# Kernel optimization log

Hardware: AMD Instinct MI355X
Metric: run time of the kernel (lower is better)

Reference implementation:

```python
import jax, jax.numpy as jnp
import numpy as np

L1_COST = 1000.0
ENTROPY_COST = 5e-05


def setup_inputs() -> dict:
    key = jax.random.key(0)
    k1, k2 = jax.random.split(key)
    inputs = jax.random.normal(k1, (8, 4096, 256), dtype=jnp.float32)
    # xavier_uniform for [K, D]: bound = sqrt(6/(K+D))
    K, D = 1024, 256
    bound = np.sqrt(6.0 / (K + D)).astype(np.float32)
    codebook = jax.random.uniform(k2, (K, D), dtype=jnp.float32, minval=-bound, maxval=bound)
    return {"inputs": inputs, "codebook": codebook}


def reference(inputs, codebook):
    D = codebook.shape[1]
    flat = inputs.reshape(-1, D)                                  # [N, D]
    norm_C = codebook / jnp.linalg.norm(codebook, axis=1, keepdims=True)   # [K, D]
    flat = flat / jnp.linalg.norm(flat, axis=1, keepdims=True)    # [N, D]
    distances = jax.nn.softmax(flat @ norm_C.T, axis=1)           # [N, K]
    reconstruction = (distances @ norm_C).reshape(inputs.shape)   # [B, S, D]
    # l1_loss(distances, zeros) == mean(|distances|)
    l1 = jnp.mean(jnp.abs(distances))
    # entropy term: mean_i sum_k [ -log_softmax(distances) @ distances.T ]_{ik}
    # = mean_i ( -log_softmax(distances)_i . colsum(distances) ), an O(N*K) equivalent
    log_sm = jax.nn.log_softmax(distances, axis=1)                # [N, K]
    col_sum = jnp.sum(distances, axis=0)                          # [K]
    entropy = jnp.mean(-(log_sm @ col_sum))
    loss = L1_COST * l1 + ENTROPY_COST * entropy
    return reconstruction, loss
```

## Files before the change

### kernel.cpp

```cpp
#include <hip/hip_runtime.h>
#include <cstdint>

#define N_ROWS 32768
#define KDIM 1024
#define DDIM 256

typedef __attribute__((ext_vector_type(8))) short bf16x8;
typedef __attribute__((ext_vector_type(4))) float f32x4;

__device__ __forceinline__ unsigned short f2bf(float f) {
  unsigned int u = __float_as_uint(f);
  u += 0x7FFFu + ((u >> 16) & 1u);
  return (unsigned short)(u >> 16);
}
__device__ __forceinline__ float bf2f(unsigned short b) {
  return __uint_as_float((unsigned int)b << 16);
}

__device__ __forceinline__ void gload_lds16(const void* g, void* l) {
  __builtin_amdgcn_global_load_lds(
      (const __attribute__((address_space(1))) unsigned int*)(uintptr_t)g,
      (__attribute__((address_space(3))) unsigned int*)(unsigned int)(uintptr_t)l,
      16, 0, 0);
}


__global__ __launch_bounds__(256) void k_norm_cb(const float* __restrict__ cb,
                                                 unsigned short* __restrict__ Cn,
                                                 unsigned short* __restrict__ CnT,
                                                 float* __restrict__ m_g) {
  __shared__ float msh[4][256];
  const int wid = threadIdx.x >> 6, lane = threadIdx.x & 63;
  const int k = blockIdx.x * 4 + wid;
  float4 v = ((const float4*)(cb + (size_t)k * DDIM))[lane];
  float s = v.x * v.x + v.y * v.y + v.z * v.z + v.w * v.w;
#pragma unroll
  for (int m = 32; m; m >>= 1) s += __shfl_xor(s, m, 64);
  const float rn = 1.0f / sqrtf(s);
  ushort4 p;
  p.x = f2bf(v.x * rn); p.y = f2bf(v.y * rn);
  p.z = f2bf(v.z * rn); p.w = f2bf(v.w * rn);
  const int kb = lane >> 3;
  const int physA = ((lane & 7) >> 1) ^ (k & 3);
  *(ushort4*)(Cn + (size_t)(k >> 6) * 16384 + kb * 2048 + (k & 63) * 32 + physA * 8 + (lane & 1) * 4) = p;
  const int sgl = k >> 5, c31 = k & 31, ch = c31 >> 3, cw = c31 & 7;
  const unsigned short pv[4] = {p.x, p.y, p.z, p.w};
#pragma unroll
  for (int j = 0; j < 4; ++j) {
    const int d = lane * 4 + j;
    CnT[(size_t)sgl * 8192 + d * 32 + ((ch ^ j) * 8) + cw] = pv[j];
    msh[wid][d] = bf2f(pv[j]);
  }
  __syncthreads();
  const int tid = threadIdx.x;
  if (tid < 256) atomicAdd(&m_g[tid], msh[0][tid] + msh[1][tid] + msh[2][tid] + msh[3][tid]);
}

__global__ __launch_bounds__(256) void k_gram(const unsigned short* __restrict__ CnT,
                                              unsigned short* __restrict__ Mn) {
  __shared__ unsigned short T[2][8192];
  const int tid = threadIdx.x, wv = tid >> 6, lane = tid & 63;
  const int l15 = lane & 15, l4 = lane >> 4;
  const int ab = blockIdx.x;
  const int xsw = l4 ^ (l15 & 3);
  f32x4 acc[4] = {};
#pragma unroll
  for (int i = 0; i < 4; ++i) {
    const int o = i * 2048 + tid * 8;
    gload_lds16(CnT + o, (char*)T[0] + (size_t)o * 2);
  }
  for (int ks = 0; ks < 32; ++ks) {
    __syncthreads();
    if (ks < 31) {
#pragma unroll
      for (int i = 0; i < 4; ++i) {
        const int o = i * 2048 + tid * 8;
        gload_lds16(CnT + (size_t)(ks + 1) * 8192 + o, (char*)T[(ks + 1) & 1] + (size_t)o * 2);
      }
    }
    const unsigned short* B = T[ks & 1];
    bf16x8 a = *(const bf16x8*)&B[(ab * 16 + l15) * 32 + xsw * 8];
#pragma unroll
    for (int ni = 0; ni < 4; ++ni) {
      const int d = wv * 64 + ni * 16 + l15;
      bf16x8 b = *(const bf16x8*)&B[d * 32 + xsw * 8];
      acc[ni] = __builtin_amdgcn_mfma_f32_16x16x32_bf16(a, b, acc[ni], 0, 0, 0);
    }
  }
#pragma unroll
  for (int ni = 0; ni < 4; ++ni)
#pragma unroll
    for (int reg = 0; reg < 4; ++reg) {
      const int a_ = ab * 16 + l4 * 4 + reg;
      const int b_ = wv * 64 + ni * 16 + l15;
      Mn[(size_t)(b_ >> 6) * 16384 + (a_ >> 5) * 2048 + (b_ & 63) * 32 +
         ((((a_ & 31) >> 3) ^ (b_ & 3)) * 8) + (a_ & 7)] = f2bf(acc[ni][reg]);
    }
}

__global__ __launch_bounds__(512, 2) void k_all(const float* __restrict__ x,
                                                const unsigned short* __restrict__ Cn,
                                                const unsigned short* __restrict__ CnT,
                                                const unsigned short* __restrict__ Mn,
                                                const float* __restrict__ m_g,
                                                float* __restrict__ colsum_g,
                                                float* __restrict__ accL,
                                                int* __restrict__ cnt2,
                                                float* __restrict__ out) {
  __shared__ unsigned short Cb[4][16384];
  __shared__ unsigned short Ps[128 * 72];
  __shared__ float csl[1024];
  __shared__ float u_sh[128], t_sh[128], irl[128];
  __shared__ float lse_sh[2];
  __shared__ float sh1[4], sh2[4];
  __shared__ int lastf;

  const int tid = threadIdx.x, wid = tid >> 6, lane = tid & 63;
  const int l15 = lane & 15, l4 = lane >> 4;
  const int wm = wid >> 1, wn = wid & 1;
  const int rb = blockIdx.x;
  if (tid < 128) t_sh[tid] = 0.f;
  for (int j = tid; j < 1024; j += 512) csl[j] = 0.f;

#define STAGE32(SRC, DST)                                          \
  do {                                                             \
    _Pragma("unroll") for (int i_ = 0; i_ < 4; ++i_) {             \
      const int off_ = i_ * 8192 + wid * 1024 + lane * 16;         \
      gload_lds16((const char*)(SRC) + off_, (char*)(DST) + off_); \
    }                                                              \
  } while (0)

  STAGE32(Mn, Cb[2]);
  STAGE32((const char*)Mn + 32768, Cb[3]);

  unsigned short* Xs = &Cb[0][0];
  const float4 mv = ((const float4*)m_g)[lane];
#pragma unroll
  for (int p16 = 0; p16 < 16; ++p16) {
    const int row = p16 * 8 + wid;
    float4 v = ((const float4*)(x + (size_t)(rb * 128 + row) * DDIM))[lane];
    float s = v.x * v.x + v.y * v.y + v.z * v.z + v.w * v.w;
#pragma unroll
    for (int m = 32; m; m >>= 1) s += __shfl_xor(s, m, 64);
    const float rn = 1.0f / sqrtf(s);
    ushort4 p;
    p.x = f2bf(v.x * rn); p.y = f2bf(v.y * rn);
    p.z = f2bf(v.z * rn); p.w = f2bf(v.w * rn);
    *(ushort4*)&Xs[(lane >> 3) * 4096 + row * 32 + (lane & 7) * 4] = p;
    float ud = bf2f(p.x) * mv.x + bf2f(p.y) * mv.y + bf2f(p.z) * mv.z + bf2f(p.w) * mv.w;
#pragma unroll
    for (int m = 32; m; m >>= 1) ud += __shfl_xor(ud, m, 64);
    if (lane == 0) u_sh[row] = ud;
  }
  __syncthreads();
  bf16x8 areg[2][8];
#pragma unroll
  for (int mi = 0; mi < 2; ++mi)
#pragma unroll
    for (int kb = 0; kb < 8; ++kb)
      areg[mi][kb] = *(const bf16x8*)&Xs[kb * 4096 + (wm * 32 + mi * 16 + l15) * 32 + l4 * 8];

  const int xsw = l4 ^ (l15 & 3);

  float tacc[2][4] = {{0.f, 0.f, 0.f, 0.f}, {0.f, 0.f, 0.f, 0.f}};
  auto t_step = [&](const unsigned short* Sm, int bbase) {
    f32x4 Y[2][2] = {};
#pragma unroll
    for (int kb = 0; kb < 8; ++kb) {
      bf16x8 b0 = *(const bf16x8*)&Sm[kb * 2048 + (wn * 32 + l15) * 32 + xsw * 8];
      bf16x8 b1 = *(const bf16x8*)&Sm[kb * 2048 + (wn * 32 + 16 + l15) * 32 + xsw * 8];
#pragma unroll
      for (int mi = 0; mi < 2; ++mi) {
        Y[mi][0] = __builtin_amdgcn_mfma_f32_16x16x32_bf16(areg[mi][kb], b0, Y[mi][0], 0, 0, 0);
        Y[mi][1] = __builtin_amdgcn_mfma_f32_16x16x32_bf16(areg[mi][kb], b1, Y[mi][1], 0, 0, 0);
      }
    }
#pragma unroll
    for (int mi = 0; mi < 2; ++mi)
#pragma unroll
      for (int ni = 0; ni < 2; ++ni) {
        const int b = bbase + wn * 32 + ni * 16 + l15;
#pragma unroll
        for (int reg = 0; reg < 4; ++reg) {
          const int row = wm * 32 + mi * 16 + l4 * 4 + reg;
          const float xv = bf2f(Xs[(b >> 5) * 4096 + row * 32 + (b & 31)]);
          tacc[mi][reg] += Y[mi][ni][reg] * xv;
        }
      }
  };
  t_step(Cb[2], 0);
  __syncthreads();
  STAGE32((const char*)Mn + 65536, Cb[2]);
  t_step(Cb[3], 64);
  __syncthreads();
  STAGE32((const char*)Mn + 98304, Cb[3]);
  t_step(Cb[2], 128);
  __syncthreads();
  STAGE32(Cn, Cb[2]);
  t_step(Cb[3], 192);
  __syncthreads();
  STAGE32(CnT, Cb[3]);

#pragma unroll
  for (int mi = 0; mi < 2; ++mi)
#pragma unroll
    for (int reg = 0; reg < 4; ++reg) {
#pragma unroll
      for (int m = 1; m < 16; m <<= 1) tacc[mi][reg] += __shfl_xor(tacc[mi][reg], m, 64);
    }
  if (l15 == 0) {
#pragma unroll
    for (int mi = 0; mi < 2; ++mi)
#pragma unroll
      for (int reg = 0; reg < 4; ++reg)
        atomicAdd(&t_sh[wm * 32 + mi * 16 + l4 * 4 + reg], tacc[mi][reg]);
  }
  __syncthreads();
  if (tid < 128) {
    const float uu = u_sh[tid], tt = t_sh[tid];
    const float r = (float)KDIM + uu + 0.5f * tt;
    const float ir = 1.0f / r;
    irl[tid] = ir;
    const float q = (float)KDIM + 2.0f * uu + 2.0f * tt;
    float lse = logf((float)(KDIM + 1) + 0.5f * q * ir * ir);
#pragma unroll
    for (int m = 32; m; m >>= 1) lse += __shfl_xor(lse, m, 64);
    if ((tid & 63) == 0) lse_sh[tid >> 6] = lse;
  }
  __syncthreads();
  if (tid == 0) atomicAdd(accL, lse_sh[0] + lse_sh[1]);
  f32x4 ir2[2];
#pragma unroll
  for (int mi = 0; mi < 2; ++mi)
    ir2[mi] = *(const f32x4*)&irl[wm * 32 + mi * 16 + l4 * 4];

  f32x4 O[2][8] = {};
  const int psw_r = l15 >> 1;
  for (int kt = 0; kt < 16; ++kt) {
    const int cslot = (kt & 1) ? 0 : 2;
    const int tslot = cslot | 1;
    const int nslot = (kt & 1) ? 2 : 0;
    if (kt < 15) STAGE32((const char*)Cn + (size_t)(kt + 1) * 32768, Cb[nslot]);
    f32x4 S[2][2] = {};
#pragma unroll
    for (int kb = 0; kb < 8; ++kb) {
      bf16x8 b[2];
#pragma unroll
      for (int ni = 0; ni < 2; ++ni)
        b[ni] = *(const bf16x8*)&Cb[cslot][kb * 2048 + (wn * 32 + ni * 16 + l15) * 32 + xsw * 8];
#pragma unroll
      for (int mi = 0; mi < 2; ++mi)
#pragma unroll
        for (int ni = 0; ni < 2; ++ni)
          S[mi][ni] = __builtin_amdgcn_mfma_f32_16x16x32_bf16(areg[mi][kb], b[ni], S[mi][ni], 0, 0, 0);
    }
    float cs[2] = {0.f, 0.f};
#pragma unroll
    for (int mi = 0; mi < 2; ++mi)
#pragma unroll
      for (int reg = 0; reg < 4; ++reg) {
        const int row = wm * 32 + mi * 16 + l4 * 4 + reg;
        const int pswz = (l4 * 2 + (reg >> 1)) & 7;
#pragma unroll
        for (int ni = 0; ni < 2; ++ni) {
          const float e = __expf(S[mi][ni][reg]);
          const int chl = wn * 4 + ni * 2 + (l15 >> 3);
          Ps[row * 72 + ((chl ^ pswz) * 8) + (l15 & 7)] = f2bf(e);
          cs[ni] += e * ir2[mi][reg];
        }
      }
#pragma unroll
    for (int ni = 0; ni < 2; ++ni) {
      float v = cs[ni];
      v += __shfl_xor(v, 16, 64);
      v += __shfl_xor(v, 32, 64);
      if (lane < 16) atomicAdd(&csl[kt * 64 + wn * 32 + ni * 16 + l15], v);
    }
    __syncthreads();
    if (kt < 15) STAGE32((const char*)CnT + (size_t)(kt + 1) * 32768, Cb[nslot + 1]);
#pragma unroll
    for (int kb2 = 0; kb2 < 2; ++kb2) {
      bf16x8 a2[2], b2[8];
#pragma unroll
      for (int mi = 0; mi < 2; ++mi) {
        const int row = wm * 32 + mi * 16 + l15;
        a2[mi] = *(const bf16x8*)&Ps[row * 72 + (((kb2 * 4 + l4) ^ psw_r) * 8)];
      }
#pragma unroll
      for (int ni = 0; ni < 8; ++ni) {
        const int d = wn * 128 + ni * 16 + l15;
        b2[ni] = *(const bf16x8*)&Cb[tslot][kb2 * 8192 + d * 32 + xsw * 8];
      }
#pragma unroll
      for (int mi = 0; mi < 2; ++mi)
#pragma unroll
        for (int ni = 0; ni < 8; ++ni)
          O[mi][ni] = __builtin_amdgcn_mfma_f32_16x16x32_bf16(a2[mi], b2[ni], O[mi][ni], 0, 0, 0);
    }
    __syncthreads();
  }

#pragma unroll
  for (int mi = 0; mi < 2; ++mi)
#pragma unroll
    for (int reg = 0; reg < 4; ++reg) {
      const int row = wm * 32 + mi * 16 + l4 * 4 + reg;
      const float irv = ir2[mi][reg];
#pragma unroll
      for (int ni = 0; ni < 8; ++ni) {
        const int d = wn * 128 + ni * 16 + l15;
        out[(size_t)(rb * 128 + row) * DDIM + d] = O[mi][ni][reg] * irv;
      }
    }
  for (int j = tid; j < 1024; j += 512) atomicAdd(&colsum_g[j], csl[j]);

  if (tid == 0) {
    __threadfence();
    const int old = __hip_atomic_fetch_add(cnt2, 1, __ATOMIC_ACQ_REL, __HIP_MEMORY_SCOPE_AGENT);
    lastf = (old == 255);
  }
  __syncthreads();
  if (lastf) {
    if (tid < 256) {
      float s = 0.f, q = 0.f;
#pragma unroll
      for (int j = 0; j < 4; ++j) {
        const float c = __hip_atomic_load(&colsum_g[tid + j * 256], __ATOMIC_RELAXED, __HIP_MEMORY_SCOPE_AGENT);
        s += c; q += c * c;
      }
#pragma unroll
      for (int m = 1; m < 64; m <<= 1) {
        s += __shfl_xor(s, m, 64);
        q += __shfl_xor(q, m, 64);
      }
      if (lane == 0) { sh1[tid >> 6] = s; sh2[tid >> 6] = q; }
    }
    __syncthreads();
    if (tid == 0) {
      const double S = (double)sh1[0] + sh1[1] + sh1[2] + sh1[3];
      const double Q = (double)sh2[0] + sh2[1] + sh2[2] + sh2[3];
      const double L = __hip_atomic_load(accL, __ATOMIC_RELAXED, __HIP_MEMORY_SCOPE_AGENT);
      const double entropy = (S * L - Q) / (double)N_ROWS;
      const double l1 = S / ((double)N_ROWS * (double)KDIM);
      out[(size_t)N_ROWS * DDIM] = (float)(1000.0 * l1 + 5e-5 * entropy);
    }
  }
#undef STAGE32
}

extern "C" void kernel_launch(void* const* d_in, const int* in_sizes, int n_in,
                              void* d_out, int out_size, void* d_ws, size_t ws_size,
                              hipStream_t stream) {
  const float* x = (const float*)d_in[0];
  const float* cb = (const float*)d_in[1];
  float* out = (float*)d_out;
  char* ws = (char*)d_ws;

  unsigned short* Cn  = (unsigned short*)(ws + 0);
  unsigned short* CnT = (unsigned short*)(ws + 524288);
  unsigned short* Mn  = (unsigned short*)(ws + 1048576);
  float* colsum_g     = (float*)(ws + 1179648);
  float* m_g          = (float*)(ws + 1183744);
  float* accL         = (float*)(ws + 1184768);
  int* cnt2           = (int*)(ws + 1184772);

  hipMemsetAsync(ws + 1179648, 0, 5128, stream);
  k_norm_cb<<<256, 256, 0, stream>>>(cb, Cn, CnT, m_g);
  k_gram<<<16, 256, 0, stream>>>(CnT, Mn);
  k_all<<<256, 512, 0, stream>>>(x, Cn, CnT, Mn, m_g, colsum_g, accL, cnt2, out);
}
```

Measured before the change: 185.2 us.

## Replace __syncthreads with partial vmcnt waits and deepen async prefetch pipelines

In the gram kernel, the LDS ring grows from two to four slots and three stages are prefetched ahead, with explicit s_waitcnt vmcnt counts so only the oldest load is awaited. In the main kernel, full __syncthreads barriers become raw s_barrier calls with targeted vmcnt/lgkmcnt waits. The CnT stage is issued together with the Cn stage one step earlier so both loads overlap the whole iteration, and the accL atomic moves to the end. This is meant to cut load stalls caused by draining all outstanding memory operations at each barrier, at the risk of race bugs if the hand-counted vmcnt values do not match the number of loads actually in flight.

Result: no change. 182.9 us (-1.2%).

```diff
diff --git a/kernel.cpp b/kernel.cpp
--- a/kernel.cpp
+++ b/kernel.cpp
@@ -58,27 +58,27 @@
 
 __global__ __launch_bounds__(256) void k_gram(const unsigned short* __restrict__ CnT,
                                               unsigned short* __restrict__ Mn) {
-  __shared__ unsigned short T[2][8192];
+  __shared__ unsigned short T[4][8192];
   const int tid = threadIdx.x, wv = tid >> 6, lane = tid & 63;
   const int l15 = lane & 15, l4 = lane >> 4;
   const int ab = blockIdx.x;
   const int xsw = l4 ^ (l15 & 3);
   f32x4 acc[4] = {};
-#pragma unroll
-  for (int i = 0; i < 4; ++i) {
-    const int o = i * 2048 + tid * 8;
-    gload_lds16(CnT + o, (char*)T[0] + (size_t)o * 2);
-  }
+#define STAGE_T(KS, SLOT)                                                            \
+  do {                                                                               \
+    _Pragma("unroll") for (int i_ = 0; i_ < 4; ++i_) {                               \
+      const int o_ = i_ * 2048 + tid * 8;                                            \
+      gload_lds16(CnT + (size_t)(KS) * 8192 + o_, (char*)T[SLOT] + (size_t)o_ * 2);  \
+    }                                                                                \
+  } while (0)
+  STAGE_T(0, 0); STAGE_T(1, 1); STAGE_T(2, 2);
   for (int ks = 0; ks < 32; ++ks) {
-    __syncthreads();
-    if (ks < 31) {
-#pragma unroll
-      for (int i = 0; i < 4; ++i) {
-        const int o = i * 2048 + tid * 8;
-        gload_lds16(CnT + (size_t)(ks + 1) * 8192 + o, (char*)T[(ks + 1) & 1] + (size_t)o * 2);
-      }
-    }
-    const unsigned short* B = T[ks & 1];
+    if (ks <= 29)      asm volatile("s_waitcnt vmcnt(8)" ::: "memory");
+    else if (ks == 30) asm volatile("s_waitcnt vmcnt(4)" ::: "memory");
+    else               asm volatile("s_waitcnt vmcnt(0)" ::: "memory");
+    __builtin_amdgcn_s_barrier();
+    __builtin_amdgcn_sched_barrier(0);
+    const unsigned short* B = T[ks & 3];
     bf16x8 a = *(const bf16x8*)&B[(ab * 16 + l15) * 32 + xsw * 8];
 #pragma unroll
     for (int ni = 0; ni < 4; ++ni) {
@@ -86,7 +86,11 @@
       bf16x8 b = *(const bf16x8*)&B[d * 32 + xsw * 8];
       acc[ni] = __builtin_amdgcn_mfma_f32_16x16x32_bf16(a, b, acc[ni], 0, 0, 0);
     }
-  }
+    __builtin_amdgcn_s_barrier();
+    __builtin_amdgcn_sched_barrier(0);
+    if (ks <= 28) STAGE_T(ks + 3, (ks + 3) & 3);
+  }
+#undef STAGE_T
 #pragma unroll
   for (int ni = 0; ni < 4; ++ni)
 #pragma unroll
@@ -189,16 +193,22 @@
       }
   };
   t_step(Cb[2], 0);
-  __syncthreads();
+  __builtin_amdgcn_s_barrier();
+  __builtin_amdgcn_sched_barrier(0);
   STAGE32((const char*)Mn + 65536, Cb[2]);
   t_step(Cb[3], 64);
-  __syncthreads();
+  asm volatile("s_waitcnt vmcnt(0)" ::: "memory");
+  __builtin_amdgcn_s_barrier();
+  __builtin_amdgcn_sched_barrier(0);
   STAGE32((const char*)Mn + 98304, Cb[3]);
   t_step(Cb[2], 128);
-  __syncthreads();
+  asm volatile("s_waitcnt vmcnt(0)" ::: "memory");
+  __builtin_amdgcn_s_barrier();
+  __builtin_amdgcn_sched_barrier(0);
   STAGE32(Cn, Cb[2]);
   t_step(Cb[3], 192);
-  __syncthreads();
+  __builtin_amdgcn_s_barrier();
+  __builtin_amdgcn_sched_barrier(0);
   STAGE32(CnT, Cb[3]);
 
 #pragma unroll
@@ -215,7 +225,8 @@
       for (int reg = 0; reg < 4; ++reg)
         atomicAdd(&t_sh[wm * 32 + mi * 16 + l4 * 4 + reg], tacc[mi][reg]);
   }
-  __syncthreads();
+  asm volatile("s_waitcnt lgkmcnt(0)" ::: "memory");
+  __builtin_amdgcn_s_barrier();
   if (tid < 128) {
     const float uu = u_sh[tid], tt = t_sh[tid];
     const float r = (float)KDIM + uu + 0.5f * tt;
@@ -227,12 +238,15 @@
     for (int m = 32; m; m >>= 1) lse += __shfl_xor(lse, m, 64);
     if ((tid & 63) == 0) lse_sh[tid >> 6] = lse;
   }
-  __syncthreads();
-  if (tid == 0) atomicAdd(accL, lse_sh[0] + lse_sh[1]);
+  asm volatile("s_waitcnt lgkmcnt(0)" ::: "memory");
+  __builtin_amdgcn_s_barrier();
   f32x4 ir2[2];
 #pragma unroll
   for (int mi = 0; mi < 2; ++mi)
     ir2[mi] = *(const f32x4*)&irl[wm * 32 + mi * 16 + l4 * 4];
+  asm volatile("s_waitcnt vmcnt(4)" ::: "memory");
+  __builtin_amdgcn_s_barrier();
+  __builtin_amdgcn_sched_barrier(0);
 
   f32x4 O[2][8] = {};
   const int psw_r = l15 >> 1;
@@ -240,7 +254,10 @@
     const int cslot = (kt & 1) ? 0 : 2;
     const int tslot = cslot | 1;
     const int nslot = (kt & 1) ? 2 : 0;
-    if (kt < 15) STAGE32((const char*)Cn + (size_t)(kt + 1) * 32768, Cb[nslot]);
+    if (kt < 15) {
+      STAGE32((const char*)Cn + (size_t)(kt + 1) * 32768, Cb[nslot]);
+      STAGE32((const char*)CnT + (size_t)(kt + 1) * 32768, Cb[nslot + 1]);
+    }
     f32x4 S[2][2] = {};
 #pragma unroll
     for (int kb = 0; kb < 8; ++kb) {
@@ -276,8 +293,10 @@
       v += __shfl_xor(v, 32, 64);
       if (lane < 16) atomicAdd(&csl[kt * 64 + wn * 32 + ni * 16 + l15], v);
     }
-    __syncthreads();
-    if (kt < 15) STAGE32((const char*)CnT + (size_t)(kt + 1) * 32768, Cb[nslot + 1]);
+    if (kt < 15) asm volatile("s_waitcnt vmcnt(8) lgkmcnt(0)" ::: "memory");
+    else         asm volatile("s_waitcnt vmcnt(0) lgkmcnt(0)" ::: "memory");
+    __builtin_amdgcn_s_barrier();
+    __builtin_amdgcn_sched_barrier(0);
 #pragma unroll
     for (int kb2 = 0; kb2 < 2; ++kb2) {
       bf16x8 a2[2], b2[8];
@@ -297,7 +316,10 @@
         for (int ni = 0; ni < 8; ++ni)
           O[mi][ni] = __builtin_amdgcn_mfma_f32_16x16x32_bf16(a2[mi], b2[ni], O[mi][ni], 0, 0, 0);
     }
-    __syncthreads();
+    if (kt < 15) asm volatile("s_waitcnt vmcnt(4)" ::: "memory");
+    else         asm volatile("s_waitcnt vmcnt(0)" ::: "memory");
+    __builtin_amdgcn_s_barrier();
+    __builtin_amdgcn_sched_barrier(0);
   }
 
 #pragma unroll
@@ -313,6 +335,7 @@
       }
     }
   for (int j = tid; j < 1024; j += 512) atomicAdd(&colsum_g[j], csl[j]);
+  if (tid == 0) atomicAdd(accL, lse_sh[0] + lse_sh[1]);
 
   if (tid == 0) {
     __threadfence();
```
